# Performance work log

Hardware: AMD Instinct MI355X
Metric: run time of the kernel (lower is better)

## Reference

```python
import jax, jax.numpy as jnp
import numpy as np

B, N, E = 4, 20000, 320000
IN_DIM, HID, OUT = 64, 128, 16


def setup_inputs() -> dict:
    key = jax.random.key(0)
    ks = jax.random.split(key, 10)
    return {
        "graph_nodes": jax.random.normal(ks[0], (B, N, IN_DIM), jnp.float32),
        "additional_features": jax.random.normal(ks[1], (B, 1), jnp.float32),
        "edge_index": jax.random.randint(ks[2], (2, E), 0, N, dtype=jnp.int32).astype(jnp.int64),
        "W1": jax.random.normal(ks[3], (IN_DIM, HID), jnp.float32) / np.sqrt(IN_DIM),
        "b1": jnp.zeros((HID,), jnp.float32),
        "W2": jax.random.normal(ks[4], (HID, HID), jnp.float32) / np.sqrt(HID),
        "b2": jnp.zeros((HID,), jnp.float32),
        "fc_w": jax.random.normal(ks[5], (HID + 1, OUT), jnp.float32) / np.sqrt(HID + 1),
        "fc_b": jnp.zeros((OUT,), jnp.float32),
        "sigma_param": jnp.zeros((OUT, 1), jnp.float32),
    }


def gcn_conv(x, src, dst, W, b, n):
    # PyG GCNConv: h = x @ W; out[dst] += deg^-1/2[src]*deg^-1/2[dst] * h[src]; out += b
    h = x @ W  # [B, N, H]
    deg = jnp.zeros((n,), h.dtype).at[dst].add(jnp.ones(dst.shape[0], h.dtype))
    dis = jax.lax.rsqrt(deg)  # self-loops guarantee deg >= 1
    norm = dis[src] * dis[dst]  # [E+N]
    msg = h[:, src, :] * norm[None, :, None]  # [B, E+N, H]
    out = jnp.zeros_like(h).at[:, dst, :].add(msg)
    return out + b


def reference(graph_nodes, additional_features, W1, b1, W2, b2, fc_w, fc_b, sigma_param, edge_index):
    n = graph_nodes.shape[1]
    loops = jnp.arange(n, dtype=edge_index.dtype)  # add_self_loops
    src = jnp.concatenate([edge_index[0], loops])
    dst = jnp.concatenate([edge_index[1], loops])
    x = jax.nn.relu(gcn_conv(graph_nodes, src, dst, W1, b1, n))
    x = jax.nn.relu(gcn_conv(x, src, dst, W2, b2, n))
    pooled = x.mean(axis=1)  # global_mean_pool (equal-size graphs)
    feats = jnp.concatenate([pooled, additional_features], axis=1)  # [B, HID+1]
    mu = feats @ fc_w + fc_b  # [B, OUT]
    sigma = jnp.exp(jnp.broadcast_to(sigma_param.reshape(1, -1), mu.shape))
    return mu, sigma
```

## Files before the change

### kernel.cpp

```cpp
#include <hip/hip_runtime.h>
#include <math.h>

#define HID 128
#define INDIM 64
#define NSH 64

typedef unsigned int uint;
typedef unsigned short ushort;
typedef __attribute__((ext_vector_type(8))) short short8;
typedef __attribute__((ext_vector_type(4))) float f32x4;

static __device__ inline float bf2f(uint h) { return __uint_as_float(h << 16); }
static __device__ inline ushort f2bf(float f) {
    uint u = __float_as_uint(f);
    return (ushort)((u + 0x7fff + ((u >> 16) & 1)) >> 16);
}
static __device__ inline uint packbf2(float a, float b) {
    return (uint)f2bf(a) | ((uint)f2bf(b) << 16);
}
static __device__ inline int imin(int a, int b) { return a < b ? a : b; }

static __device__ inline void init8(float* a, uint4 v, float sl) {
    a[0] = bf2f(v.x & 0xffffu) * sl; a[1] = bf2f(v.x >> 16) * sl;
    a[2] = bf2f(v.y & 0xffffu) * sl; a[3] = bf2f(v.y >> 16) * sl;
    a[4] = bf2f(v.z & 0xffffu) * sl; a[5] = bf2f(v.z >> 16) * sl;
    a[6] = bf2f(v.w & 0xffffu) * sl; a[7] = bf2f(v.w >> 16) * sl;
}
static __device__ inline void acc8(float* a, uint4 u, float f) {
    a[0] = fmaf(bf2f(u.x & 0xffffu), f, a[0]); a[1] = fmaf(bf2f(u.x >> 16), f, a[1]);
    a[2] = fmaf(bf2f(u.y & 0xffffu), f, a[2]); a[3] = fmaf(bf2f(u.y >> 16), f, a[3]);
    a[4] = fmaf(bf2f(u.z & 0xffffu), f, a[4]); a[5] = fmaf(bf2f(u.z >> 16), f, a[5]);
    a[6] = fmaf(bf2f(u.w & 0xffffu), f, a[6]); a[7] = fmaf(bf2f(u.w >> 16), f, a[7]);
}
static __device__ inline void init4(float* a, uint2 v, float sl) {
    a[0] = bf2f(v.x & 0xffffu) * sl; a[1] = bf2f(v.x >> 16) * sl;
    a[2] = bf2f(v.y & 0xffffu) * sl; a[3] = bf2f(v.y >> 16) * sl;
}
static __device__ inline void acc4(float* a, uint2 u, float f) {
    a[0] = fmaf(bf2f(u.x & 0xffffu), f, a[0]); a[1] = fmaf(bf2f(u.x >> 16), f, a[1]);
    a[2] = fmaf(bf2f(u.y & 0xffffu), f, a[2]); a[3] = fmaf(bf2f(u.y >> 16), f, a[3]);
}

__global__ __launch_bounds__(256) void k_init_cast(
    const float* __restrict__ x, const float* __restrict__ W1, const float* __restrict__ W2,
    const int* __restrict__ ei,
    uint* __restrict__ xbf, uint* __restrict__ w1t, uint* __restrict__ w2t,
    int* cnt, float* pooledS, int* flag, int N)
{
    int gid = blockIdx.x * 256 + threadIdx.x;
    int stride = gridDim.x * 256;
    if (blockIdx.x == 0) {
        __shared__ int sbad;
        if (threadIdx.x == 0) sbad = 0;
        __syncthreads();
        int bad = (ei[2 * threadIdx.x + 1] != 0) ? 1 : 0;
        if (__any(bad) && (threadIdx.x & 63) == 0) atomicOr(&sbad, 1);
        __syncthreads();
        if (threadIdx.x == 0) *flag = sbad;
    }
    int total = N * 128;
    for (int i = gid; i < total; i += stride) {
        int n = i >> 7, r = i & 127;
        int b = r >> 5, c2 = r & 31;
        const float* s = x + ((size_t)b * N + n) * 64 + c2 * 2;
        xbf[i] = packbf2(s[0], s[1]);
    }
    if (gid < 128 * 32) { int c = gid >> 5, k2 = gid & 31; w1t[gid] = packbf2(W1[(2 * k2) * 128 + c], W1[(2 * k2 + 1) * 128 + c]); }
    if (gid < 128 * 64) { int c = gid >> 6, k2 = gid & 63; w2t[gid] = packbf2(W2[(2 * k2) * 128 + c], W2[(2 * k2 + 1) * 128 + c]); }
    if (gid < N) cnt[gid] = 0;
    if (gid < NSH * 512) pooledS[gid] = 0.f;
}

__global__ __launch_bounds__(256) void k_edges(const int* __restrict__ ei, const int* __restrict__ flag,
                                               int* __restrict__ src, int* __restrict__ dst,
                                               int* cnt, int E) {
    int e = blockIdx.x * 256 + threadIdx.x;
    if (e >= E) return;
    int s, d;
    if (*flag) { s = ei[e]; d = ei[(size_t)E + e]; }
    else       { s = ei[2 * (size_t)e]; d = ei[2 * (size_t)E + 2 * (size_t)e]; }
    src[e] = s; dst[e] = d;
    atomicAdd(&cnt[d], 1);
}

__global__ __launch_bounds__(1024) void k_scan(const int* __restrict__ cnt, int* __restrict__ row_ptr,
                                               float* __restrict__ dis, int* __restrict__ fillcnt, int N) {
    __shared__ int wsum[16];
    int t = threadIdx.x;
    int chunk = (N + 1023) >> 10;
    int lo = t * chunk; if (lo > N) lo = N;
    int hi = lo + chunk; if (hi > N) hi = N;
    int s = 0;
#pragma unroll 4
    for (int i = lo; i < hi; i++) s += cnt[i];
    int lane = t & 63, wid = t >> 6;
    int v = s;
#pragma unroll
    for (int d = 1; d < 64; d <<= 1) {
        int u = __shfl_up(v, d);
        if (lane >= d) v += u;
    }
    if (lane == 63) wsum[wid] = v;
    __syncthreads();
    if (wid == 0) {
        int wv = (lane < 16) ? wsum[lane] : 0;
#pragma unroll
        for (int d = 1; d < 16; d <<= 1) {
            int u = __shfl_up(wv, d);
            if (lane >= d) wv += u;
        }
        if (lane < 16) wsum[lane] = wv;
    }
    __syncthreads();
    int base = (wid > 0 ? wsum[wid - 1] : 0) + (v - s);
    int acc = base;
#pragma unroll 4
    for (int i = lo; i < hi; i++) {
        row_ptr[i] = acc;
        int c = cnt[i];
        acc += c;
        dis[i] = rsqrtf((float)(c + 1));
        fillcnt[i] = 0;
    }
    if (t == 0) row_ptr[N] = wsum[15];
}

__global__ __launch_bounds__(256) void k_fill(const int* __restrict__ src, const int* __restrict__ dst,
                                              const int* __restrict__ row_ptr, int* fillcnt,
                                              int* __restrict__ col, float* __restrict__ wsrc,
                                              const float* __restrict__ dis, int E) {
    int e = blockIdx.x * 256 + threadIdx.x;
    if (e >= E) return;
    int d = dst[e], s = src[e];
    int p = row_ptr[d] + atomicAdd(&fillcnt[d], 1);
    col[p] = s;
    wsrc[p] = dis[s];
}

__global__ __launch_bounds__(256, 4) void k_l1(
    const uint* __restrict__ xbf, const int* __restrict__ rp, const int* __restrict__ col,
    const float* __restrict__ wsrc, const float* __restrict__ dis,
    const uint* __restrict__ w1t, const float* __restrict__ b1,
    uint* __restrict__ x1, int ntile)
{
    __shared__ __align__(16) char sW[16384];
    __shared__ __align__(16) char sXa[4][2048];
    int t = threadIdx.x, w = t >> 6, l = t & 63;
    int g = l >> 4, row = l & 15;
    for (int i = t; i < 1024; i += 256) {
        int c = i >> 3, ch = i & 7;
        *(uint4*)(sW + c * 128 + ((ch ^ (c & 7)) << 4)) = *(const uint4*)(w1t + c * 32 + ch * 4);
    }
    __syncthreads();
    int tile = blockIdx.x * 4 + w;
    if (tile >= ntile) return;
    char* sX = sXa[w];
    const uint2* xr = (const uint2*)xbf;

    int n0 = tile * 4;
    int r0 = rp[n0], r1 = rp[n0 + 1], r2 = rp[n0 + 2], r3 = rp[n0 + 3], r4 = rp[n0 + 4];
    int e0 = r0, e1 = r1, e2 = r2, e3 = r3;
    float dn0 = dis[n0], dn1 = dis[n0 + 1], dn2 = dis[n0 + 2], dn3 = dis[n0 + 3];
    float ac0[4], ac1[4], ac2[4], ac3[4];
    init4(ac0, xr[(size_t)n0 * 64 + l], dn0 * dn0);
    init4(ac1, xr[(size_t)(n0 + 1) * 64 + l], dn1 * dn1);
    init4(ac2, xr[(size_t)(n0 + 2) * 64 + l], dn2 * dn2);
    init4(ac3, xr[(size_t)(n0 + 3) * 64 + l], dn3 * dn3);

#define A2(j) do { \
    int c0_ = col[e##j], c1_ = col[e##j + 1]; \
    float f0_ = wsrc[e##j] * dn##j, f1_ = wsrc[e##j + 1] * dn##j; \
    uint2 u0_ = xr[(size_t)c0_ * 64 + l], u1_ = xr[(size_t)c1_ * 64 + l]; \
    acc4(ac##j, u0_, f0_); acc4(ac##j, u1_, f1_); e##j += 2; } while (0)
#define A1(j) do { \
    int c0_ = col[e##j]; float f0_ = wsrc[e##j] * dn##j; \
    uint2 u0_ = xr[(size_t)c0_ * 64 + l]; acc4(ac##j, u0_, f0_); e##j += 1; } while (0)

    int m = imin(imin(r1 - e0, r2 - e1), imin(r3 - e2, r4 - e3)) >> 1;
    for (int it = 0; it < m; it++) { A2(0); A2(1); A2(2); A2(3); }
    int p01 = imin(r1 - e0, r2 - e1) >> 1;
    for (int it = 0; it < p01; it++) { A2(0); A2(1); }
    int p23 = imin(r3 - e2, r4 - e3) >> 1;
    for (int it = 0; it < p23; it++) { A2(2); A2(3); }
    while (e0 + 1 < r1) A2(0);
    if (e0 < r1) A1(0);
    while (e1 + 1 < r2) A2(1);
    if (e1 < r2) A1(1);
    while (e2 + 1 < r3) A2(2);
    if (e2 < r3) A1(2);
    while (e3 + 1 < r4) A2(3);
    if (e3 < r4) A1(3);
#undef A2
#undef A1

    {
        uint2 pk;
        pk.x = packbf2(ac0[0], ac0[1]); pk.y = packbf2(ac0[2], ac0[3]);
        int wr = g;
        *(uint2*)(sX + wr * 128 + (((row >> 1) ^ (wr & 7)) << 4) + ((row & 1) << 3)) = pk;
        pk.x = packbf2(ac1[0], ac1[1]); pk.y = packbf2(ac1[2], ac1[3]);
        wr = 4 + g;
        *(uint2*)(sX + wr * 128 + (((row >> 1) ^ (wr & 7)) << 4) + ((row & 1) << 3)) = pk;
        pk.x = packbf2(ac2[0], ac2[1]); pk.y = packbf2(ac2[2], ac2[3]);
        wr = 8 + g;
        *(uint2*)(sX + wr * 128 + (((row >> 1) ^ (wr & 7)) << 4) + ((row & 1) << 3)) = pk;
        pk.x = packbf2(ac3[0], ac3[1]); pk.y = packbf2(ac3[2], ac3[3]);
        wr = 12 + g;
        *(uint2*)(sX + wr * 128 + (((row >> 1) ^ (wr & 7)) << 4) + ((row & 1) << 3)) = pk;
    }
    int ro0 = row * 128 + ((g ^ (row & 7)) << 4);
    int ro1 = row * 128 + (((4 + g) ^ (row & 7)) << 4);
    short8 xf0 = *(const short8*)(sX + ro0);
    short8 xf1 = *(const short8*)(sX + ro1);
    size_t rbase = ((size_t)tile * 16 + row) * 32;
#pragma unroll
    for (int q = 0; q < 8; q++) {
        f32x4 a = {0.f, 0.f, 0.f, 0.f};
        const char* wb = sW + q * 2048;
        a = __builtin_amdgcn_mfma_f32_16x16x32_bf16(*(const short8*)(wb + ro0), xf0, a, 0, 0, 0);
        a = __builtin_amdgcn_mfma_f32_16x16x32_bf16(*(const short8*)(wb + ro1), xf1, a, 0, 0, 0);
        float4 bb = *(const float4*)(b1 + q * 16 + g * 4);
        uint2 o;
        o.x = packbf2(fmaxf(a.x + bb.x, 0.f), fmaxf(a.y + bb.y, 0.f));
        o.y = packbf2(fmaxf(a.z + bb.z, 0.f), fmaxf(a.w + bb.w, 0.f));
        ((uint2*)x1)[rbase + q * 4 + g] = o;
    }
}

__global__ __launch_bounds__(256, 3) void k_l2(
    const uint* __restrict__ x1, const int* __restrict__ rp, const int* __restrict__ col,
    const float* __restrict__ wsrc, const float* __restrict__ dis,
    const uint* __restrict__ w2t, const float* __restrict__ b2,
    float* __restrict__ pooledS, int ntile, float invN)
{
    __shared__ __align__(16) char sW[32768];
    __shared__ __align__(16) char sXa[4][4096];
    int t = threadIdx.x, w = t >> 6, l = t & 63;
    int g = l >> 4, row = l & 15;
    for (int i = t; i < 2048; i += 256) {
        int c = i >> 4, ch = i & 15;
        *(uint4*)(sW + c * 256 + ((ch ^ (c & 7)) << 4)) = *(const uint4*)(w2t + c * 64 + ch * 4);
    }
    __syncthreads();
    int tile = blockIdx.x * 4 + w;
    if (tile >= ntile) return;
    char* sX = sXa[w];
    const uint4* xr = (const uint4*)x1;

    int n0 = tile * 4;
    int r0 = rp[n0], r1 = rp[n0 + 1], r2 = rp[n0 + 2], r3 = rp[n0 + 3], r4 = rp[n0 + 4];
    int e0 = r0, e1 = r1, e2 = r2, e3 = r3;
    float dn0 = dis[n0], dn1 = dis[n0 + 1], dn2 = dis[n0 + 2], dn3 = dis[n0 + 3];
    float ac0[8], ac1[8], ac2[8], ac3[8];
    init8(ac0, xr[(size_t)n0 * 64 + l], dn0 * dn0);
    init8(ac1, xr[(size_t)(n0 + 1) * 64 + l], dn1 * dn1);
    init8(ac2, xr[(size_t)(n0 + 2) * 64 + l], dn2 * dn2);
    init8(ac3, xr[(size_t)(n0 + 3) * 64 + l], dn3 * dn3);

#define B2(j) do { \
    int c0_ = col[e##j], c1_ = col[e##j + 1]; \
    float f0_ = wsrc[e##j] * dn##j, f1_ = wsrc[e##j + 1] * dn##j; \
    uint4 u0_ = xr[(size_t)c0_ * 64 + l], u1_ = xr[(size_t)c1_ * 64 + l]; \
    acc8(ac##j, u0_, f0_); acc8(ac##j, u1_, f1_); e##j += 2; } while (0)
#define B1(j) do { \
    int c0_ = col[e##j]; float f0_ = wsrc[e##j] * dn##j; \
    uint4 u0_ = xr[(size_t)c0_ * 64 + l]; acc8(ac##j, u0_, f0_); e##j += 1; } while (0)

    int m = imin(imin(r1 - e0, r2 - e1), imin(r3 - e2, r4 - e3)) >> 1;
    for (int it = 0; it < m; it++) { B2(0); B2(1); B2(2); B2(3); }
    int p01 = imin(r1 - e0, r2 - e1) >> 1;
    for (int it = 0; it < p01; it++) { B2(0); B2(1); }
    int p23 = imin(r3 - e2, r4 - e3) >> 1;
    for (int it = 0; it < p23; it++) { B2(2); B2(3); }
    while (e0 + 1 < r1) B2(0);
    if (e0 < r1) B1(0);
    while (e1 + 1 < r2) B2(1);
    if (e1 < r2) B1(1);
    while (e2 + 1 < r3) B2(2);
    if (e2 < r3) B1(2);
    while (e3 + 1 < r4) B2(3);
    if (e3 < r4) B1(3);
#undef B2
#undef B1

    {
        uint4 pk;
        pk.x = packbf2(ac0[0], ac0[1]); pk.y = packbf2(ac0[2], ac0[3]);
        pk.z = packbf2(ac0[4], ac0[5]); pk.w = packbf2(ac0[6], ac0[7]);
        int wr = g;
        *(uint4*)(sX + wr * 256 + ((row ^ (wr & 7)) << 4)) = pk;
        pk.x = packbf2(ac1[0], ac1[1]); pk.y = packbf2(ac1[2], ac1[3]);
        pk.z = packbf2(ac1[4], ac1[5]); pk.w = packbf2(ac1[6], ac1[7]);
        wr = 4 + g;
        *(uint4*)(sX + wr * 256 + ((row ^ (wr & 7)) << 4)) = pk;
        pk.x = packbf2(ac2[0], ac2[1]); pk.y = packbf2(ac2[2], ac2[3]);
        pk.z = packbf2(ac2[4], ac2[5]); pk.w = packbf2(ac2[6], ac2[7]);
        wr = 8 + g;
        *(uint4*)(sX + wr * 256 + ((row ^ (wr & 7)) << 4)) = pk;
        pk.x = packbf2(ac3[0], ac3[1]); pk.y = packbf2(ac3[2], ac3[3]);
        pk.z = packbf2(ac3[4], ac3[5]); pk.w = packbf2(ac3[6], ac3[7]);
        wr = 12 + g;
        *(uint4*)(sX + wr * 256 + ((row ^ (wr & 7)) << 4)) = pk;
    }
    int ro0 = row * 256 + ((g ^ (row & 7)) << 4);
    int ro1 = row * 256 + (((4 + g) ^ (row & 7)) << 4);
    int ro2 = row * 256 + (((8 + g) ^ (row & 7)) << 4);
    int ro3 = row * 256 + (((12 + g) ^ (row & 7)) << 4);
    short8 xf0 = *(const short8*)(sX + ro0);
    short8 xf1 = *(const short8*)(sX + ro1);
    short8 xf2 = *(const short8*)(sX + ro2);
    short8 xf3 = *(const short8*)(sX + ro3);
#pragma unroll
    for (int q = 0; q < 8; q++) {
        f32x4 a = {0.f, 0.f, 0.f, 0.f};
        const char* wb = sW + q * 4096;
        a = __builtin_amdgcn_mfma_f32_16x16x32_bf16(*(const short8*)(wb + ro0), xf0, a, 0, 0, 0);
        a = __builtin_amdgcn_mfma_f32_16x16x32_bf16(*(const short8*)(wb + ro1), xf1, a, 0, 0, 0);
        a = __builtin_amdgcn_mfma_f32_16x16x32_bf16(*(const short8*)(wb + ro2), xf2, a, 0, 0, 0);
        a = __builtin_amdgcn_mfma_f32_16x16x32_bf16(*(const short8*)(wb + ro3), xf3, a, 0, 0, 0);
        float4 bb = *(const float4*)(b2 + q * 16 + g * 4);
        float v0 = fmaxf(a.x + bb.x, 0.f);
        float v1 = fmaxf(a.y + bb.y, 0.f);
        float v2 = fmaxf(a.z + bb.z, 0.f);
        float v3 = fmaxf(a.w + bb.w, 0.f);
        v0 += __shfl_xor(v0, 4); v0 += __shfl_xor(v0, 8);
        v1 += __shfl_xor(v1, 4); v1 += __shfl_xor(v1, 8);
        v2 += __shfl_xor(v2, 4); v2 += __shfl_xor(v2, 8);
        v3 += __shfl_xor(v3, 4); v3 += __shfl_xor(v3, 8);
        if ((l & 12) == 0) {
            float* pd = pooledS + (size_t)(tile & (NSH - 1)) * 512 + (l & 3) * 128 + q * 16 + g * 4;
            atomicAdd(pd + 0, v0 * invN);
            atomicAdd(pd + 1, v1 * invN);
            atomicAdd(pd + 2, v2 * invN);
            atomicAdd(pd + 3, v3 * invN);
        }
    }
}

__global__ __launch_bounds__(512) void k_head(const float* __restrict__ pooledS, const float* __restrict__ af,
                                              const float* __restrict__ fcw, const float* __restrict__ fcb,
                                              const float* __restrict__ sig, float* __restrict__ out, int B) {
    __shared__ float pool[512];
    int t = threadIdx.x;
    float s = 0.f;
#pragma unroll 8
    for (int sh = 0; sh < NSH; sh++) s += pooledS[sh * 512 + t];
    pool[t] = s;
    __syncthreads();
    if (t >= B * 16) return;
    int b = t >> 4, o = t & 15;
    float acc = fcb[o];
    for (int c = 0; c < HID; c++) acc = fmaf(pool[b * 128 + c], fcw[c * 16 + o], acc);
    acc = fmaf(af[b], fcw[HID * 16 + o], acc);
    out[t] = acc;
    out[B * 16 + t] = expf(sig[o]);
}


extern "C" void kernel_launch(void* const* d_in, const int* in_sizes, int n_in,
                              void* d_out, int out_size, void* d_ws, size_t ws_size,
                              hipStream_t stream) {
    const float* x   = (const float*)d_in[0];
    const float* af  = (const float*)d_in[1];
    const int*   ei  = (const int*)d_in[2];
    const float* W1  = (const float*)d_in[3];
    const float* b1  = (const float*)d_in[4];
    const float* W2  = (const float*)d_in[5];
    const float* b2  = (const float*)d_in[6];
    const float* fcw = (const float*)d_in[7];
    const float* fcb = (const float*)d_in[8];
    const float* sig = (const float*)d_in[9];

    int B = in_sizes[1];
    int E = in_sizes[2] / 2;
    int N = in_sizes[0] / (B * INDIM);
    int ntile = N / 4;

    char* p = (char*)d_ws;
    auto alloc = [&](size_t bytes) { void* r = (void*)p; p += (bytes + 255) & ~(size_t)255; return r; };
    int*    cnt     = (int*)alloc((size_t)N * 4);
    int*    fillcnt = (int*)alloc((size_t)N * 4);
    int*    row_ptr = (int*)alloc((size_t)(N + 1) * 4);
    int*    colA    = (int*)alloc((size_t)E * 4);
    int*    srcA    = (int*)alloc((size_t)E * 4);
    int*    dstA    = (int*)alloc((size_t)E * 4);
    float*  wsrcA   = (float*)alloc((size_t)E * 4);
    float*  dis     = (float*)alloc((size_t)N * 4);
    float*  pooledS = (float*)alloc((size_t)NSH * 512 * 4);
    int*    flag    = (int*)alloc(256);
    uint*   xbf     = (uint*)alloc((size_t)N * 128 * 4);
    uint*   x1      = (uint*)alloc((size_t)N * 4 * 64 * 4);
    uint*   w1t     = (uint*)alloc((size_t)128 * 32 * 4);
    uint*   w2t     = (uint*)alloc((size_t)128 * 64 * 4);
    (void)ws_size;

    int gE = (E + 255) / 256;
    int gL = (ntile + 3) / 4;

    k_init_cast<<<2048, 256, 0, stream>>>(x, W1, W2, ei, xbf, w1t, w2t, cnt, pooledS, flag, N);
    k_edges<<<gE, 256, 0, stream>>>(ei, flag, srcA, dstA, cnt, E);
    k_scan<<<1, 1024, 0, stream>>>(cnt, row_ptr, dis, fillcnt, N);
    k_fill<<<gE, 256, 0, stream>>>(srcA, dstA, row_ptr, fillcnt, colA, wsrcA, dis, E);

    k_l1<<<gL, 256, 0, stream>>>(xbf, row_ptr, colA, wsrcA, dis, w1t, b1, x1, ntile);
    k_l2<<<gL, 256, 0, stream>>>(x1, row_ptr, colA, wsrcA, dis, w2t, b2, pooledS, ntile, 1.0f / (float)N);

    k_head<<<1, 512, 0, stream>>>(pooledS, af, fcw, fcb, sig, (float*)d_out, B);
}
```

Measured before the change: 179.7 us.

## Switch node features to batch-major layout and per-batch tiles in GCN layers

Stores bf16 node features batch-major, so each gathered row is one batch's feature vector, and maps blocks to (batch, 16-node tile) pairs. Each 16-lane group now walks one node's neighbour list, with the loop bound set to the maximum across groups, instead of the old four-node interleaved unrolling. Layer 2 drops its shared-memory W2 staging and reads weights straight from global memory to allow higher occupancy. Gathers are narrower (32 or 64 bytes per row per batch) and the same edges are reread for each batch, which trades gather efficiency for locality and occupancy, and divergent degrees waste lanes.

Result: slower. 201.7 us (+12.3%).

```diff
diff --git a/kernel.cpp b/kernel.cpp
--- a/kernel.cpp
+++ b/kernel.cpp
@@ -18,7 +18,7 @@
 static __device__ inline uint packbf2(float a, float b) {
     return (uint)f2bf(a) | ((uint)f2bf(b) << 16);
 }
-static __device__ inline int imin(int a, int b) { return a < b ? a : b; }
+static __device__ inline int imax(int a, int b) { return a > b ? a : b; }
 
 static __device__ inline void init8(float* a, uint4 v, float sl) {
     a[0] = bf2f(v.x & 0xffffu) * sl; a[1] = bf2f(v.x >> 16) * sl;
@@ -59,12 +59,8 @@
         if (threadIdx.x == 0) *flag = sbad;
     }
     int total = N * 128;
-    for (int i = gid; i < total; i += stride) {
-        int n = i >> 7, r = i & 127;
-        int b = r >> 5, c2 = r & 31;
-        const float* s = x + ((size_t)b * N + n) * 64 + c2 * 2;
-        xbf[i] = packbf2(s[0], s[1]);
-    }
+    for (int i = gid; i < total; i += stride)
+        xbf[i] = packbf2(x[2 * (size_t)i], x[2 * (size_t)i + 1]);
     if (gid < 128 * 32) { int c = gid >> 5, k2 = gid & 31; w1t[gid] = packbf2(W1[(2 * k2) * 128 + c], W1[(2 * k2 + 1) * 128 + c]); }
     if (gid < 128 * 64) { int c = gid >> 6, k2 = gid & 63; w2t[gid] = packbf2(W2[(2 * k2) * 128 + c], W2[(2 * k2 + 1) * 128 + c]); }
     if (gid < N) cnt[gid] = 0;
@@ -137,11 +133,18 @@
     wsrc[p] = dis[s];
 }
 
+#define BATCH_MAP() \
+    int bid = blockIdx.x; \
+    int bq = (bid & 7) >> 1; \
+    int jj = ((bid >> 3) << 1) | (bid & 1); \
+    int tl = jj * 4 + w; \
+    if (tl >= ntiles) return;
+
 __global__ __launch_bounds__(256, 4) void k_l1(
     const uint* __restrict__ xbf, const int* __restrict__ rp, const int* __restrict__ col,
     const float* __restrict__ wsrc, const float* __restrict__ dis,
     const uint* __restrict__ w1t, const float* __restrict__ b1,
-    uint* __restrict__ x1, int ntile)
+    uint* __restrict__ x1, int N, int ntiles)
 {
     __shared__ __align__(16) char sW[16384];
     __shared__ __align__(16) char sXa[4][2048];
@@ -152,67 +155,40 @@
         *(uint4*)(sW + c * 128 + ((ch ^ (c & 7)) << 4)) = *(const uint4*)(w1t + c * 32 + ch * 4);
     }
     __syncthreads();
-    int tile = blockIdx.x * 4 + w;
-    if (tile >= ntile) return;
+    BATCH_MAP();
     char* sX = sXa[w];
-    const uint2* xr = (const uint2*)xbf;
-
-    int n0 = tile * 4;
-    int r0 = rp[n0], r1 = rp[n0 + 1], r2 = rp[n0 + 2], r3 = rp[n0 + 3], r4 = rp[n0 + 4];
-    int e0 = r0, e1 = r1, e2 = r2, e3 = r3;
-    float dn0 = dis[n0], dn1 = dis[n0 + 1], dn2 = dis[n0 + 2], dn3 = dis[n0 + 3];
-    float ac0[4], ac1[4], ac2[4], ac3[4];
-    init4(ac0, xr[(size_t)n0 * 64 + l], dn0 * dn0);
-    init4(ac1, xr[(size_t)(n0 + 1) * 64 + l], dn1 * dn1);
-    init4(ac2, xr[(size_t)(n0 + 2) * 64 + l], dn2 * dn2);
-    init4(ac3, xr[(size_t)(n0 + 3) * 64 + l], dn3 * dn3);
-
-#define A2(j) do { \
-    int c0_ = col[e##j], c1_ = col[e##j + 1]; \
-    float f0_ = wsrc[e##j] * dn##j, f1_ = wsrc[e##j + 1] * dn##j; \
-    uint2 u0_ = xr[(size_t)c0_ * 64 + l], u1_ = xr[(size_t)c1_ * 64 + l]; \
-    acc4(ac##j, u0_, f0_); acc4(ac##j, u1_, f1_); e##j += 2; } while (0)
-#define A1(j) do { \
-    int c0_ = col[e##j]; float f0_ = wsrc[e##j] * dn##j; \
-    uint2 u0_ = xr[(size_t)c0_ * 64 + l]; acc4(ac##j, u0_, f0_); e##j += 1; } while (0)
-
-    int m = imin(imin(r1 - e0, r2 - e1), imin(r3 - e2, r4 - e3)) >> 1;
-    for (int it = 0; it < m; it++) { A2(0); A2(1); A2(2); A2(3); }
-    int p01 = imin(r1 - e0, r2 - e1) >> 1;
-    for (int it = 0; it < p01; it++) { A2(0); A2(1); }
-    int p23 = imin(r3 - e2, r4 - e3) >> 1;
-    for (int it = 0; it < p23; it++) { A2(2); A2(3); }
-    while (e0 + 1 < r1) A2(0);
-    if (e0 < r1) A1(0);
-    while (e1 + 1 < r2) A2(1);
-    if (e1 < r2) A1(1);
-    while (e2 + 1 < r3) A2(2);
-    if (e2 < r3) A1(2);
-    while (e3 + 1 < r4) A2(3);
-    if (e3 < r4) A1(3);
-#undef A2
-#undef A1
-
-    {
-        uint2 pk;
-        pk.x = packbf2(ac0[0], ac0[1]); pk.y = packbf2(ac0[2], ac0[3]);
-        int wr = g;
-        *(uint2*)(sX + wr * 128 + (((row >> 1) ^ (wr & 7)) << 4) + ((row & 1) << 3)) = pk;
-        pk.x = packbf2(ac1[0], ac1[1]); pk.y = packbf2(ac1[2], ac1[3]);
-        wr = 4 + g;
-        *(uint2*)(sX + wr * 128 + (((row >> 1) ^ (wr & 7)) << 4) + ((row & 1) << 3)) = pk;
-        pk.x = packbf2(ac2[0], ac2[1]); pk.y = packbf2(ac2[2], ac2[3]);
-        wr = 8 + g;
-        *(uint2*)(sX + wr * 128 + (((row >> 1) ^ (wr & 7)) << 4) + ((row & 1) << 3)) = pk;
-        pk.x = packbf2(ac3[0], ac3[1]); pk.y = packbf2(ac3[2], ac3[3]);
-        wr = 12 + g;
-        *(uint2*)(sX + wr * 128 + (((row >> 1) ^ (wr & 7)) << 4) + ((row & 1) << 3)) = pk;
+    const uint2* xb = (const uint2*)xbf + (size_t)bq * N * 16;
+    int n0 = tl * 16;
+
+#pragma unroll
+    for (int p = 0; p < 4; p++) {
+        int node = n0 + p * 4 + g;
+        float dn = dis[node];
+        int beg = rp[node], end = rp[node + 1];
+        int len = end - beg;
+        float ac[4];
+        init4(ac, xb[(size_t)node * 16 + row], dn * dn);
+        int mx = len;
+        mx = imax(mx, __shfl_xor(mx, 16));
+        mx = imax(mx, __shfl_xor(mx, 32));
+        for (int i = 0; i < mx; i += 2) {
+            int e0 = beg + i, e1 = e0 + 1;
+            bool a0 = i < len, a1 = i + 1 < len;
+            uint2 u0, u1; float f0 = 0.f, f1 = 0.f;
+            if (a0) { int s = col[e0]; f0 = wsrc[e0] * dn; u0 = xb[(size_t)s * 16 + row]; }
+            if (a1) { int s = col[e1]; f1 = wsrc[e1] * dn; u1 = xb[(size_t)s * 16 + row]; }
+            if (a0) acc4(ac, u0, f0);
+            if (a1) acc4(ac, u1, f1);
+        }
+        int r = p * 4 + g;
+        uint2 pk; pk.x = packbf2(ac[0], ac[1]); pk.y = packbf2(ac[2], ac[3]);
+        *(uint2*)(sX + r * 128 + (((row >> 1) ^ (r & 7)) << 4) + ((row & 1) << 3)) = pk;
     }
     int ro0 = row * 128 + ((g ^ (row & 7)) << 4);
     int ro1 = row * 128 + (((4 + g) ^ (row & 7)) << 4);
     short8 xf0 = *(const short8*)(sX + ro0);
     short8 xf1 = *(const short8*)(sX + ro1);
-    size_t rbase = ((size_t)tile * 16 + row) * 32;
+    size_t rbase = ((size_t)bq * N + n0 + row) * 32;
 #pragma unroll
     for (int q = 0; q < 8; q++) {
         f32x4 a = {0.f, 0.f, 0.f, 0.f};
@@ -227,112 +203,74 @@
     }
 }
 
-__global__ __launch_bounds__(256, 3) void k_l2(
+__global__ __launch_bounds__(256, 6) void k_l2(
     const uint* __restrict__ x1, const int* __restrict__ rp, const int* __restrict__ col,
     const float* __restrict__ wsrc, const float* __restrict__ dis,
     const uint* __restrict__ w2t, const float* __restrict__ b2,
-    float* __restrict__ pooledS, int ntile, float invN)
+    float* __restrict__ pooledS, int N, int ntiles, float invN)
 {
-    __shared__ __align__(16) char sW[32768];
     __shared__ __align__(16) char sXa[4][4096];
     int t = threadIdx.x, w = t >> 6, l = t & 63;
     int g = l >> 4, row = l & 15;
-    for (int i = t; i < 2048; i += 256) {
-        int c = i >> 4, ch = i & 15;
-        *(uint4*)(sW + c * 256 + ((ch ^ (c & 7)) << 4)) = *(const uint4*)(w2t + c * 64 + ch * 4);
-    }
-    __syncthreads();
-    int tile = blockIdx.x * 4 + w;
-    if (tile >= ntile) return;
+    BATCH_MAP();
     char* sX = sXa[w];
-    const uint4* xr = (const uint4*)x1;
-
-    int n0 = tile * 4;
-    int r0 = rp[n0], r1 = rp[n0 + 1], r2 = rp[n0 + 2], r3 = rp[n0 + 3], r4 = rp[n0 + 4];
-    int e0 = r0, e1 = r1, e2 = r2, e3 = r3;
-    float dn0 = dis[n0], dn1 = dis[n0 + 1], dn2 = dis[n0 + 2], dn3 = dis[n0 + 3];
-    float ac0[8], ac1[8], ac2[8], ac3[8];
-    init8(ac0, xr[(size_t)n0 * 64 + l], dn0 * dn0);
-    init8(ac1, xr[(size_t)(n0 + 1) * 64 + l], dn1 * dn1);
-    init8(ac2, xr[(size_t)(n0 + 2) * 64 + l], dn2 * dn2);
-    init8(ac3, xr[(size_t)(n0 + 3) * 64 + l], dn3 * dn3);
-
-#define B2(j) do { \
-    int c0_ = col[e##j], c1_ = col[e##j + 1]; \
-    float f0_ = wsrc[e##j] * dn##j, f1_ = wsrc[e##j + 1] * dn##j; \
-    uint4 u0_ = xr[(size_t)c0_ * 64 + l], u1_ = xr[(size_t)c1_ * 64 + l]; \
-    acc8(ac##j, u0_, f0_); acc8(ac##j, u1_, f1_); e##j += 2; } while (0)
-#define B1(j) do { \
-    int c0_ = col[e##j]; float f0_ = wsrc[e##j] * dn##j; \
-    uint4 u0_ = xr[(size_t)c0_ * 64 + l]; acc8(ac##j, u0_, f0_); e##j += 1; } while (0)
-
-    int m = imin(imin(r1 - e0, r2 - e1), imin(r3 - e2, r4 - e3)) >> 1;
-    for (int it = 0; it < m; it++) { B2(0); B2(1); B2(2); B2(3); }
-    int p01 = imin(r1 - e0, r2 - e1) >> 1;
-    for (int it = 0; it < p01; it++) { B2(0); B2(1); }
-    int p23 = imin(r3 - e2, r4 - e3) >> 1;
-    for (int it = 0; it < p23; it++) { B2(2); B2(3); }
-    while (e0 + 1 < r1) B2(0);
-    if (e0 < r1) B1(0);
-    while (e1 + 1 < r2) B2(1);
-    if (e1 < r2) B1(1);
-    while (e2 + 1 < r3) B2(2);
-    if (e2 < r3) B1(2);
-    while (e3 + 1 < r4) B2(3);
-    if (e3 < r4) B1(3);
-#undef B2
-#undef B1
-
-    {
+    const uint4* xb = (const uint4*)x1 + (size_t)bq * N * 16;
+    int n0 = tl * 16;
+
+#pragma unroll
+    for (int p = 0; p < 4; p++) {
+        int node = n0 + p * 4 + g;
+        float dn = dis[node];
+        int beg = rp[node], end = rp[node + 1];
+        int len = end - beg;
+        float ac[8];
+        init8(ac, xb[(size_t)node * 16 + row], dn * dn);
+        int mx = len;
+        mx = imax(mx, __shfl_xor(mx, 16));
+        mx = imax(mx, __shfl_xor(mx, 32));
+        for (int i = 0; i < mx; i += 2) {
+            int e0 = beg + i, e1 = e0 + 1;
+            bool a0 = i < len, a1 = i + 1 < len;
+            uint4 u0, u1; float f0 = 0.f, f1 = 0.f;
+            if (a0) { int s = col[e0]; f0 = wsrc[e0] * dn; u0 = xb[(size_t)s * 16 + row]; }
+            if (a1) { int s = col[e1]; f1 = wsrc[e1] * dn; u1 = xb[(size_t)s * 16 + row]; }
+            if (a0) acc8(ac, u0, f0);
+            if (a1) acc8(ac, u1, f1);
+        }
+        int r = p * 4 + g;
         uint4 pk;
-        pk.x = packbf2(ac0[0], ac0[1]); pk.y = packbf2(ac0[2], ac0[3]);
-        pk.z = packbf2(ac0[4], ac0[5]); pk.w = packbf2(ac0[6], ac0[7]);
-        int wr = g;
-        *(uint4*)(sX + wr * 256 + ((row ^ (wr & 7)) << 4)) = pk;
-        pk.x = packbf2(ac1[0], ac1[1]); pk.y = packbf2(ac1[2], ac1[3]);
-        pk.z = packbf2(ac1[4], ac1[5]); pk.w = packbf2(ac1[6], ac1[7]);
-        wr = 4 + g;
-        *(uint4*)(sX + wr * 256 + ((row ^ (wr & 7)) << 4)) = pk;
-        pk.x = packbf2(ac2[0], ac2[1]); pk.y = packbf2(ac2[2], ac2[3]);
-        pk.z = packbf2(ac2[4], ac2[5]); pk.w = packbf2(ac2[6], ac2[7]);
-        wr = 8 + g;
-        *(uint4*)(sX + wr * 256 + ((row ^ (wr & 7)) << 4)) = pk;
-        pk.x = packbf2(ac3[0], ac3[1]); pk.y = packbf2(ac3[2], ac3[3]);
-        pk.z = packbf2(ac3[4], ac3[5]); pk.w = packbf2(ac3[6], ac3[7]);
-        wr = 12 + g;
-        *(uint4*)(sX + wr * 256 + ((row ^ (wr & 7)) << 4)) = pk;
-    }
-    int ro0 = row * 256 + ((g ^ (row & 7)) << 4);
-    int ro1 = row * 256 + (((4 + g) ^ (row & 7)) << 4);
-    int ro2 = row * 256 + (((8 + g) ^ (row & 7)) << 4);
-    int ro3 = row * 256 + (((12 + g) ^ (row & 7)) << 4);
-    short8 xf0 = *(const short8*)(sX + ro0);
-    short8 xf1 = *(const short8*)(sX + ro1);
-    short8 xf2 = *(const short8*)(sX + ro2);
-    short8 xf3 = *(const short8*)(sX + ro3);
-#pragma unroll
+        pk.x = packbf2(ac[0], ac[1]); pk.y = packbf2(ac[2], ac[3]);
+        pk.z = packbf2(ac[4], ac[5]); pk.w = packbf2(ac[6], ac[7]);
+        *(uint4*)(sX + r * 256 + ((row ^ (r & 7)) << 4)) = pk;
+    }
+    short8 xf[4];
+#pragma unroll
+    for (int ks = 0; ks < 4; ks++)
+        xf[ks] = *(const short8*)(sX + row * 256 + (((ks * 4 + g) ^ (row & 7)) << 4));
+    int sh = tl & (NSH - 1);
+    float* pd = pooledS + (size_t)sh * 512 + bq * 128;
+#pragma unroll 2
     for (int q = 0; q < 8; q++) {
+        const uint* wq = w2t + (q * 16 + row) * 64 + g * 4;
         f32x4 a = {0.f, 0.f, 0.f, 0.f};
-        const char* wb = sW + q * 4096;
-        a = __builtin_amdgcn_mfma_f32_16x16x32_bf16(*(const short8*)(wb + ro0), xf0, a, 0, 0, 0);
-        a = __builtin_amdgcn_mfma_f32_16x16x32_bf16(*(const short8*)(wb + ro1), xf1, a, 0, 0, 0);
-        a = __builtin_amdgcn_mfma_f32_16x16x32_bf16(*(const short8*)(wb + ro2), xf2, a, 0, 0, 0);
-        a = __builtin_amdgcn_mfma_f32_16x16x32_bf16(*(const short8*)(wb + ro3), xf3, a, 0, 0, 0);
+        a = __builtin_amdgcn_mfma_f32_16x16x32_bf16(*(const short8*)(wq),      xf[0], a, 0, 0, 0);
+        a = __builtin_amdgcn_mfma_f32_16x16x32_bf16(*(const short8*)(wq + 16), xf[1], a, 0, 0, 0);
+        a = __builtin_amdgcn_mfma_f32_16x16x32_bf16(*(const short8*)(wq + 32), xf[2], a, 0, 0, 0);
+        a = __builtin_amdgcn_mfma_f32_16x16x32_bf16(*(const short8*)(wq + 48), xf[3], a, 0, 0, 0);
         float4 bb = *(const float4*)(b2 + q * 16 + g * 4);
         float v0 = fmaxf(a.x + bb.x, 0.f);
         float v1 = fmaxf(a.y + bb.y, 0.f);
         float v2 = fmaxf(a.z + bb.z, 0.f);
         float v3 = fmaxf(a.w + bb.w, 0.f);
-        v0 += __shfl_xor(v0, 4); v0 += __shfl_xor(v0, 8);
-        v1 += __shfl_xor(v1, 4); v1 += __shfl_xor(v1, 8);
-        v2 += __shfl_xor(v2, 4); v2 += __shfl_xor(v2, 8);
-        v3 += __shfl_xor(v3, 4); v3 += __shfl_xor(v3, 8);
-        if ((l & 12) == 0) {
-            float* pd = pooledS + (size_t)(tile & (NSH - 1)) * 512 + (l & 3) * 128 + q * 16 + g * 4;
-            atomicAdd(pd + 0, v0 * invN);
-            atomicAdd(pd + 1, v1 * invN);
-            atomicAdd(pd + 2, v2 * invN);
-            atomicAdd(pd + 3, v3 * invN);
+        v0 += __shfl_xor(v0, 1); v0 += __shfl_xor(v0, 2); v0 += __shfl_xor(v0, 4); v0 += __shfl_xor(v0, 8);
+        v1 += __shfl_xor(v1, 1); v1 += __shfl_xor(v1, 2); v1 += __shfl_xor(v1, 4); v1 += __shfl_xor(v1, 8);
+        v2 += __shfl_xor(v2, 1); v2 += __shfl_xor(v2, 2); v2 += __shfl_xor(v2, 4); v2 += __shfl_xor(v2, 8);
+        v3 += __shfl_xor(v3, 1); v3 += __shfl_xor(v3, 2); v3 += __shfl_xor(v3, 4); v3 += __shfl_xor(v3, 8);
+        if (row == 0) {
+            atomicAdd(&pd[q * 16 + g * 4 + 0], v0 * invN);
+            atomicAdd(&pd[q * 16 + g * 4 + 1], v1 * invN);
+            atomicAdd(&pd[q * 16 + g * 4 + 2], v2 * invN);
+            atomicAdd(&pd[q * 16 + g * 4 + 3], v3 * invN);
         }
     }
 }
@@ -374,7 +312,7 @@
     int B = in_sizes[1];
     int E = in_sizes[2] / 2;
     int N = in_sizes[0] / (B * INDIM);
-    int ntile = N / 4;
+    int ntiles = N / 16;
 
     char* p = (char*)d_ws;
     auto alloc = [&](size_t bytes) { void* r = (void*)p; p += (bytes + 255) & ~(size_t)255; return r; };
@@ -395,15 +333,15 @@
     (void)ws_size;
 
     int gE = (E + 255) / 256;
-    int gL = (ntile + 3) / 4;
+    int gL = 8 * ((((ntiles + 3) / 4) + 1) / 2);
 
     k_init_cast<<<2048, 256, 0, stream>>>(x, W1, W2, ei, xbf, w1t, w2t, cnt, pooledS, flag, N);
     k_edges<<<gE, 256, 0, stream>>>(ei, flag, srcA, dstA, cnt, E);
     k_scan<<<1, 1024, 0, stream>>>(cnt, row_ptr, dis, fillcnt, N);
     k_fill<<<gE, 256, 0, stream>>>(srcA, dstA, row_ptr, fillcnt, colA, wsrcA, dis, E);
 
-    k_l1<<<gL, 256, 0, stream>>>(xbf, row_ptr, colA, wsrcA, dis, w1t, b1, x1, ntile);
-    k_l2<<<gL, 256, 0, stream>>>(x1, row_ptr, colA, wsrcA, dis, w2t, b2, pooledS, ntile, 1.0f / (float)N);
+    k_l1<<<gL, 256, 0, stream>>>(xbf, row_ptr, colA, wsrcA, dis, w1t, b1, x1, N, ntiles);
+    k_l2<<<gL, 256, 0, stream>>>(x1, row_ptr, colA, wsrcA, dis, w2t, b2, pooledS, N, ntiles, 1.0f / (float)N);
 
     k_head<<<1, 512, 0, stream>>>(pooledS, af, fcw, fcb, sig, (float*)d_out, B);
 }
```
